# Performance work log

Hardware: AMD Instinct MI355X
Metric: run time of the kernel (lower is better)

## Reference

```python
import jax, jax.numpy as jnp
import numpy as np

B, N = 1024, 4096
EPS = 1e-4


def setup_inputs() -> dict:
    key = jax.random.key(0)
    k1, k2, k3 = jax.random.split(key, 3)
    src_coords = jax.random.normal(k1, (B, N, 2), dtype=jnp.float32)
    tgt_coords = jax.random.normal(k2, (B, N, 2), dtype=jnp.float32)
    weights = jax.random.uniform(k3, (B, 1, N), dtype=jnp.float32)
    return {"src_coords": src_coords, "tgt_coords": tgt_coords, "weights": weights}


def reference(src_coords, tgt_coords, weights):
    # pad 2D -> 3D (z = 0), matching F.pad(..., [0, pad, 0, 0])
    src = jnp.pad(src_coords, ((0, 0), (0, 0), (0, 1)))  # [B, N, 3]
    tgt = jnp.pad(tgt_coords, ((0, 0), (0, 0), (0, 1)))
    src = src.transpose(0, 2, 1)  # [B, 3, N]
    tgt = tgt.transpose(0, 2, 1)

    w = jnp.sum(weights, axis=2, keepdims=True) + EPS          # [B, 1, 1]
    src_centroid = jnp.sum(src * weights, axis=2, keepdims=True) / w  # [B, 3, 1]
    tgt_centroid = jnp.sum(tgt * weights, axis=2, keepdims=True) / w
    src_centered = src - src_centroid
    tgt_centered = tgt - tgt_centroid

    # weighted cross-covariance: [B, 3, 3]
    W = jnp.einsum('bin,bjn->bij', tgt_centered * weights, src_centered) / w

    U, _, Vh = jnp.linalg.svd(W)  # torch.svd returns V; V^T == Vh
    det_UV = jnp.linalg.det(U) * jnp.linalg.det(Vh)  # det(V) == det(Vh)
    ones = jnp.ones((W.shape[0],), dtype=W.dtype)
    s_diag = jnp.stack([ones, ones, det_UV], axis=1)  # [B, 3]
    # R = U @ diag(s) @ Vh
    R_tgt_src = jnp.einsum('bij,bj,bjk->bik', U, s_diag, Vh)

    t_tgt_src_insrc = src_centroid - jnp.einsum('bji,bjk->bik', R_tgt_src, tgt_centroid)
    t_src_tgt_intgt = -jnp.einsum('bij,bjk->bik', R_tgt_src, t_tgt_src_insrc)
    return (R_tgt_src, t_src_tgt_intgt)
```

## Files before the change

### kernel.cpp

```cpp
#include <hip/hip_runtime.h>


constexpr int BATCH = 1024;
constexpr int NPTS  = 4096;
constexpr double EPSV = 1e-4;

__device__ __forceinline__ double wredd(double v) {
    #pragma unroll
    for (int off = 1; off < 64; off <<= 1) v += __shfl_xor(v, off, 64);
    return v;
}

__global__ __launch_bounds__(256) void procrustes_kernel(
    const float* __restrict__ src, const float* __restrict__ tgt,
    const float* __restrict__ wts, float* __restrict__ out)
{
    const int b   = blockIdx.x;
    const int tid = threadIdx.x;
    const float* sb = src + (size_t)b * (NPTS * 2);
    const float* tb = tgt + (size_t)b * (NPTS * 2);
    const float* wb = wts + (size_t)b * NPTS;

    double acc[9] = {0,0,0,0,0,0,0,0,0};

    #pragma unroll
    for (int pass = 0; pass < NPTS / 1024; ++pass) {
        const int i = tid * 4 + pass * 1024;
        const float4 wv  = *reinterpret_cast<const float4*>(wb + i);
        const float4 sa  = *reinterpret_cast<const float4*>(sb + 2 * i);
        const float4 sc  = *reinterpret_cast<const float4*>(sb + 2 * i + 4);
        const float4 ta  = *reinterpret_cast<const float4*>(tb + 2 * i);
        const float4 tc  = *reinterpret_cast<const float4*>(tb + 2 * i + 4);

        const float wf[4] = {wv.x, wv.y, wv.z, wv.w};
        const float sxf[4] = {sa.x, sa.z, sc.x, sc.z};
        const float syf[4] = {sa.y, sa.w, sc.y, sc.w};
        const float txf[4] = {ta.x, ta.z, tc.x, tc.z};
        const float tyf[4] = {ta.y, ta.w, tc.y, tc.w};

        #pragma unroll
        for (int j = 0; j < 4; ++j) {
            const double w  = (double)wf[j];
            const double sx = (double)sxf[j], sy = (double)syf[j];
            const double tx = (double)txf[j], ty = (double)tyf[j];
            acc[0] += w;
            acc[1] = fma(w, sx, acc[1]);
            acc[2] = fma(w, sy, acc[2]);
            acc[3] = fma(w, tx, acc[3]);
            acc[4] = fma(w, ty, acc[4]);
            const double wt0 = w * tx, wt1 = w * ty;
            acc[5] = fma(wt0, sx, acc[5]);
            acc[6] = fma(wt0, sy, acc[6]);
            acc[7] = fma(wt1, sx, acc[7]);
            acc[8] = fma(wt1, sy, acc[8]);
        }
    }

    #pragma unroll
    for (int k = 0; k < 9; ++k) acc[k] = wredd(acc[k]);

    __shared__ double red[4][9];
    const int lane = tid & 63, wave = tid >> 6;
    if (lane == 0) {
        #pragma unroll
        for (int k = 0; k < 9; ++k) red[wave][k] = acc[k];
    }
    __syncthreads();

    if (tid == 0) {
        double s[9];
        #pragma unroll
        for (int k = 0; k < 9; ++k)
            s[k] = red[0][k] + red[1][k] + red[2][k] + red[3][k];

        const double w   = s[0] + EPSV;
        const double inv = 1.0 / w;
        const double scx = s[1] * inv, scy = s[2] * inv;
        const double tcx = s[3] * inv, tcy = s[4] * inv;

        const double a00 = s[5] - s[3] * s[1] * inv;
        const double a01 = s[6] - s[3] * s[2] * inv;
        const double a10 = s[7] - s[4] * s[1] * inv;
        const double a11 = s[8] - s[4] * s[2] * inv;

        const double p = 0.5 * (a00 + a11);
        const double q = 0.5 * (a10 - a01);
        const double r = 0.5 * (a00 - a11);
        const double t = 0.5 * (a01 + a10);

        const double rot2 = p * p + q * q;
        const double ref2 = r * r + t * t;

        double R00, R01, R10, R11, Rzz;
        if (rot2 >= ref2) {
            const double n = rsqrt(fmax(rot2, 1e-300));
            R00 =  p * n; R01 = -q * n;
            R10 =  q * n; R11 =  p * n;
            Rzz = 1.0;
        } else {
            const double n = rsqrt(fmax(ref2, 1e-300));
            R00 =  r * n; R01 =  t * n;
            R10 =  t * n; R11 = -r * n;
            Rzz = -1.0;
        }

        const double t1x = scx - (R00 * tcx + R10 * tcy);
        const double t1y = scy - (R01 * tcx + R11 * tcy);
        const double t2x = -(R00 * t1x + R01 * t1y);
        const double t2y = -(R10 * t1x + R11 * t1y);

        float* Ro = out + (size_t)b * 9;
        Ro[0] = (float)R00; Ro[1] = (float)R01; Ro[2] = 0.0f;
        Ro[3] = (float)R10; Ro[4] = (float)R11; Ro[5] = 0.0f;
        Ro[6] = 0.0f;       Ro[7] = 0.0f;       Ro[8] = (float)Rzz;

        float* To = out + (size_t)BATCH * 9 + (size_t)b * 3;
        To[0] = (float)t2x; To[1] = (float)t2y; To[2] = 0.0f;
    }
}

extern "C" void kernel_launch(void* const* d_in, const int* in_sizes, int n_in,
                              void* d_out, int out_size, void* d_ws, size_t ws_size,
                              hipStream_t stream) {
    const float* src = (const float*)d_in[0];
    const float* tgt = (const float*)d_in[1];
    const float* wts = (const float*)d_in[2];
    float* out = (float*)d_out;
    procrustes_kernel<<<BATCH, 256, 0, stream>>>(src, tgt, wts, out);
}
```

Measured before the change: 102.8 us.

## Split per-batch moment reduction across four blocks with separate solve kernel

Each batch's 4096 points are now reduced by four blocks, each handling a 1024-point slice and writing nine double partial sums to the workspace. A second small kernel combines the four partials and solves the 2D Procrustes rotation and translation. The aim is more blocks in flight and more memory parallelism on the bandwidth-bound reduction. The cost is a second kernel launch, a workspace round trip, and less work per thread, so less latency hiding within each block.

```diff
diff --git a/kernel.cpp b/kernel.cpp
--- a/kernel.cpp
+++ b/kernel.cpp
@@ -3,6 +3,7 @@
 
 constexpr int BATCH = 1024;
 constexpr int NPTS  = 4096;
+constexpr int SLICES = 4;
 constexpr double EPSV = 1e-4;
 
 __device__ __forceinline__ double wredd(double v) {
@@ -11,49 +12,48 @@
     return v;
 }
 
-__global__ __launch_bounds__(256) void procrustes_kernel(
+__global__ __launch_bounds__(256) void moments_kernel(
     const float* __restrict__ src, const float* __restrict__ tgt,
-    const float* __restrict__ wts, float* __restrict__ out)
+    const float* __restrict__ wts, double* __restrict__ partial)
 {
-    const int b   = blockIdx.x;
-    const int tid = threadIdx.x;
+    const int blk   = blockIdx.x;
+    const int b     = blk >> 2;
+    const int slice = blk & 3;
+    const int tid   = threadIdx.x;
+
+    const int i = slice * 1024 + tid * 4;
     const float* sb = src + (size_t)b * (NPTS * 2);
     const float* tb = tgt + (size_t)b * (NPTS * 2);
     const float* wb = wts + (size_t)b * NPTS;
 
+    const float4 wv = *reinterpret_cast<const float4*>(wb + i);
+    const float4 sa = *reinterpret_cast<const float4*>(sb + 2 * i);
+    const float4 sc = *reinterpret_cast<const float4*>(sb + 2 * i + 4);
+    const float4 ta = *reinterpret_cast<const float4*>(tb + 2 * i);
+    const float4 tc = *reinterpret_cast<const float4*>(tb + 2 * i + 4);
+
+    const float wf[4]  = {wv.x, wv.y, wv.z, wv.w};
+    const float sxf[4] = {sa.x, sa.z, sc.x, sc.z};
+    const float syf[4] = {sa.y, sa.w, sc.y, sc.w};
+    const float txf[4] = {ta.x, ta.z, tc.x, tc.z};
+    const float tyf[4] = {ta.y, ta.w, tc.y, tc.w};
+
     double acc[9] = {0,0,0,0,0,0,0,0,0};
-
     #pragma unroll
-    for (int pass = 0; pass < NPTS / 1024; ++pass) {
-        const int i = tid * 4 + pass * 1024;
-        const float4 wv  = *reinterpret_cast<const float4*>(wb + i);
-        const float4 sa  = *reinterpret_cast<const float4*>(sb + 2 * i);
-        const float4 sc  = *reinterpret_cast<const float4*>(sb + 2 * i + 4);
-        const float4 ta  = *reinterpret_cast<const float4*>(tb + 2 * i);
-        const float4 tc  = *reinterpret_cast<const float4*>(tb + 2 * i + 4);
-
-        const float wf[4] = {wv.x, wv.y, wv.z, wv.w};
-        const float sxf[4] = {sa.x, sa.z, sc.x, sc.z};
-        const float syf[4] = {sa.y, sa.w, sc.y, sc.w};
-        const float txf[4] = {ta.x, ta.z, tc.x, tc.z};
-        const float tyf[4] = {ta.y, ta.w, tc.y, tc.w};
-
-        #pragma unroll
-        for (int j = 0; j < 4; ++j) {
-            const double w  = (double)wf[j];
-            const double sx = (double)sxf[j], sy = (double)syf[j];
-            const double tx = (double)txf[j], ty = (double)tyf[j];
-            acc[0] += w;
-            acc[1] = fma(w, sx, acc[1]);
-            acc[2] = fma(w, sy, acc[2]);
-            acc[3] = fma(w, tx, acc[3]);
-            acc[4] = fma(w, ty, acc[4]);
-            const double wt0 = w * tx, wt1 = w * ty;
-            acc[5] = fma(wt0, sx, acc[5]);
-            acc[6] = fma(wt0, sy, acc[6]);
-            acc[7] = fma(wt1, sx, acc[7]);
-            acc[8] = fma(wt1, sy, acc[8]);
-        }
+    for (int j = 0; j < 4; ++j) {
+        const double w  = (double)wf[j];
+        const double sx = (double)sxf[j], sy = (double)syf[j];
+        const double tx = (double)txf[j], ty = (double)tyf[j];
+        acc[0] += w;
+        acc[1] = fma(w, sx, acc[1]);
+        acc[2] = fma(w, sy, acc[2]);
+        acc[3] = fma(w, tx, acc[3]);
+        acc[4] = fma(w, ty, acc[4]);
+        const double wt0 = w * tx, wt1 = w * ty;
+        acc[5] = fma(wt0, sx, acc[5]);
+        acc[6] = fma(wt0, sy, acc[6]);
+        acc[7] = fma(wt1, sx, acc[7]);
+        acc[8] = fma(wt1, sy, acc[8]);
     }
 
     #pragma unroll
@@ -67,12 +67,30 @@
     }
     __syncthreads();
 
-    if (tid == 0) {
-        double s[9];
+    if (tid < 9) {
+        const int k = tid;
+        partial[(size_t)blk * 9 + k] =
+            red[0][k] + red[1][k] + red[2][k] + red[3][k];
+    }
+}
+
+__global__ __launch_bounds__(64) void solve_kernel(
+    const double* __restrict__ partial, float* __restrict__ out)
+{
+    const int b    = blockIdx.x;
+    const int lane = threadIdx.x;
+
+    __shared__ double s[9];
+    if (lane < 9) {
+        double v = 0.0;
         #pragma unroll
-        for (int k = 0; k < 9; ++k)
-            s[k] = red[0][k] + red[1][k] + red[2][k] + red[3][k];
+        for (int j = 0; j < SLICES; ++j)
+            v += partial[((size_t)b * SLICES + j) * 9 + lane];
+        s[lane] = v;
+    }
+    __syncthreads();
 
+    if (lane == 0) {
         const double w   = s[0] + EPSV;
         const double inv = 1.0 / w;
         const double scx = s[1] * inv, scy = s[2] * inv;
@@ -126,5 +144,8 @@
     const float* tgt = (const float*)d_in[1];
     const float* wts = (const float*)d_in[2];
     float* out = (float*)d_out;
-    procrustes_kernel<<<BATCH, 256, 0, stream>>>(src, tgt, wts, out);
+    double* partial = (double*)d_ws;
+
+    moments_kernel<<<BATCH * SLICES, 256, 0, stream>>>(src, tgt, wts, partial);
+    solve_kernel<<<BATCH, 64, 0, stream>>>(partial, out);
 }
```

Result: slower. 111.6 us (+8.5%).
